# Optimization experiments

Measured on AMD Instinct MI355X. Metric: run time of the kernel, lower is better.

## Reference

```python
import jax, jax.numpy as jnp
import numpy as np

EPS = 1e-5  # BatchNorm3d default eps


def conv1x1(x, w, b):
    # x: (b, cin, t, h, w); w: (cout, cin); b: (cout,)
    return jnp.einsum('bcthw,oc->bothw', x, w) + b[None, :, None, None, None]


def batchnorm(x):
    # BatchNorm3d(affine=False), training mode: per-channel batch stats over (B,T,H,W)
    mean = jnp.mean(x, axis=(0, 2, 3, 4), keepdims=True)
    var = jnp.var(x, axis=(0, 2, 3, 4), keepdims=True)
    return (x - mean) * jax.lax.rsqrt(var + EPS)


def setup_inputs() -> dict:
    key = jax.random.key(0)
    ks = jax.random.split(key, 9)
    B, C, T, H, W = 4, 512, 16, 14, 14
    IC = C // 4
    s_in = 1.0 / np.sqrt(C)
    s_up = 1.0 / np.sqrt(IC)
    return {
        'maps':    jax.random.normal(ks[0], (B, C, T, H, W), jnp.float32),
        'w_theta': jax.random.uniform(ks[1], (IC, C), jnp.float32, -s_in, s_in),
        'b_theta': jax.random.uniform(ks[2], (IC,),   jnp.float32, -s_in, s_in),
        'w_phalt': jax.random.uniform(ks[3], (IC, C), jnp.float32, -s_in, s_in),
        'b_phalt': jax.random.uniform(ks[4], (IC,),   jnp.float32, -s_in, s_in),
        'w_glob':  jax.random.uniform(ks[5], (IC, C), jnp.float32, -s_in, s_in),
        'b_glob':  jax.random.uniform(ks[6], (IC,),   jnp.float32, -s_in, s_in),
        'w_up':    jax.random.uniform(ks[7], (C, IC), jnp.float32, -s_up, s_up),
        'b_up':    jax.random.uniform(ks[8], (C,),    jnp.float32, -s_up, s_up),
    }


def reference(maps, w_theta, b_theta, w_phalt, b_phalt, w_glob, b_glob, w_up, b_up):
    b, c, t, h, w = maps.shape
    ic = c // 4
    n = t * h * w

    theta_maps = batchnorm(conv1x1(maps, w_theta, b_theta))   # (b, ic, t, h, w)
    phalt_maps = batchnorm(conv1x1(maps, w_phalt, b_phalt))   # computed but UNUSED (bug in original)
    global_maps = batchnorm(conv1x1(maps, w_glob, b_glob))

    theta_x = theta_maps.reshape(b, ic, n)                    # (b, ic, n)
    # NOTE: original code uses theta_maps for phalt_x (faithful to source bug)
    relation = jnp.einsum('bcn,bcm->bnm', theta_x, theta_x)   # (b, n, n)
    relation_normalize = jax.nn.softmax(relation / n, axis=-1)

    global_x = global_maps.reshape(b, ic, n)                  # (b, ic, n)
    y = jnp.einsum('bnm,bcm->bcn', relation_normalize, global_x)
    y = y.reshape(b, ic, t, h, w)

    out = conv1x1(y, w_up, b_up) + maps
    return out
```

## Files before the change

kernel.cpp:

```cpp
#include <hip/hip_runtime.h>
#include <hip/hip_bf16.h>


typedef __attribute__((ext_vector_type(8))) short bf16x8;
typedef __attribute__((ext_vector_type(4))) float f32x4;
typedef __attribute__((ext_vector_type(16))) float f32x16;
typedef __attribute__((ext_vector_type(4))) short s16x4;

#define NTOK 3136
#define NELEM 1605632
#define NSPLIT 4

__device__ inline float bf2f(short u) {
    union { unsigned int i; float f; } v;
    v.i = ((unsigned int)(unsigned short)u) << 16;
    return v.f;
}
__device__ inline short f2bf(float x) {
    union { float f; unsigned int i; } v;
    v.f = x;
    unsigned int r = v.i + 0x7FFFu + ((v.i >> 16) & 1u);
    return (short)(r >> 16);
}
__device__ inline unsigned pk2(float lo, float hi) {
    union { float f; unsigned u; } a, b;
    a.f = lo; b.f = hi;
    return __builtin_amdgcn_perm(b.u, a.u, 0x07060302u);
}
__device__ inline void pl32swap(unsigned &a, unsigned &b) {
    asm("v_permlane32_swap_b32 %0, %1" : "+v"(a), "+v"(b));
}
__device__ inline void glds16(const void* g, void* l) {
    __builtin_amdgcn_global_load_lds((const __attribute__((address_space(1))) void*)g,
                                     (__attribute__((address_space(3))) void*)l, 16, 0, 0);
}

__global__ __launch_bounds__(256) void prep_w(const float* __restrict__ wt,
                                              const float* __restrict__ wg,
                                              const float* __restrict__ wup,
                                              short* __restrict__ Wb,
                                              short* __restrict__ wupb)
{
    const int i = blockIdx.x * 256 + threadIdx.x;
    if (i < 131072) {
        const int r = i >> 9;
        const int c = i & 511;
        const float w = (r < 128) ? wt[(size_t)r * 512 + c] : wg[(size_t)(r - 128) * 512 + c];
        Wb[i] = f2bf(w);
    } else {
        const int j = i - 131072;
        wupb[j] = f2bf(wup[j]);
    }
}

__global__ __launch_bounds__(256) void conv_in_f(const float* __restrict__ maps,
                                                 const short* __restrict__ Wb,
                                                 short* __restrict__ Tt,
                                                 short* __restrict__ Gpre,
                                                 float* __restrict__ psum,
                                                 float* __restrict__ psq)
{
    const int nt = blockIdx.x, b = blockIdx.y;
    const int n0 = nt * 32;
    const int t = threadIdx.x;
    const int w = __builtin_amdgcn_readfirstlane(t >> 6);
    const int lane = t & 63;
    const int l15 = lane & 15, lhi = lane >> 4;

    __shared__ short Bt[32][136];

    const float* mp = maps + (size_t)b * 512 * NTOK + n0;
    const int cl = t >> 3;
    const int f4 = t & 7;

    f32x4 acc[4][2];
#pragma unroll
    for (int g = 0; g < 4; g++)
#pragma unroll
        for (int j = 0; j < 2; j++) acc[g][j] = f32x4{0.f, 0.f, 0.f, 0.f};

    f32x4 rg[4];
#pragma unroll
    for (int p = 0; p < 4; p++)
        rg[p] = *(const f32x4*)(mp + (size_t)(p * 32 + cl) * NTOK + f4 * 4);

    for (int kc = 0; kc < 4; kc++) {
        __syncthreads();
#pragma unroll
        for (int p = 0; p < 4; p++) {
            const int cc = p * 32 + cl;
#pragma unroll
            for (int i = 0; i < 4; i++) Bt[f4 * 4 + i][cc] = f2bf(rg[p][i]);
        }
        if (kc < 3) {
#pragma unroll
            for (int p = 0; p < 4; p++)
                rg[p] = *(const f32x4*)(mp + (size_t)((kc + 1) * 128 + p * 32 + cl) * NTOK + f4 * 4);
        }
        __syncthreads();
#pragma unroll
        for (int ks = 0; ks < 4; ks++) {
            bf16x8 af[4], bv[2];
#pragma unroll
            for (int g = 0; g < 4; g++)
                af[g] = *(const bf16x8*)(Wb + (size_t)(w * 64 + g * 16 + l15) * 512 + kc * 128 + ks * 32 + lhi * 8);
#pragma unroll
            for (int j = 0; j < 2; j++)
                bv[j] = *(const bf16x8*)(&Bt[j * 16 + l15][ks * 32 + lhi * 8]);
#pragma unroll
            for (int g = 0; g < 4; g++)
#pragma unroll
                for (int j = 0; j < 2; j++)
                    acc[g][j] = __builtin_amdgcn_mfma_f32_16x16x32_bf16(af[g], bv[j], acc[g][j], 0, 0, 0);
        }
    }

    if (w < 2) {
#pragma unroll
        for (int g = 0; g < 4; g++)
#pragma unroll
            for (int j = 0; j < 2; j++) {
                s16x4 v;
#pragma unroll
                for (int r = 0; r < 4; r++) v[r] = f2bf(acc[g][j][r]);
                *(s16x4*)(Tt + ((size_t)b * NTOK + n0 + j * 16 + l15) * 128 + w * 64 + g * 16 + lhi * 4) = v;
            }
    } else {
#pragma unroll
        for (int g = 0; g < 4; g++)
#pragma unroll
            for (int j = 0; j < 2; j++)
#pragma unroll
                for (int r = 0; r < 4; r++) {
                    const int icg = (w - 2) * 64 + g * 16 + lhi * 4 + r;
                    Gpre[((size_t)b * 128 + icg) * NTOK + n0 + j * 16 + l15] = f2bf(acc[g][j][r]);
                }
    }
#pragma unroll
    for (int g = 0; g < 4; g++)
#pragma unroll
        for (int r = 0; r < 4; r++) {
            float s = acc[g][0][r] + acc[g][1][r];
            float q = acc[g][0][r] * acc[g][0][r] + acc[g][1][r] * acc[g][1][r];
#pragma unroll
            for (int off = 1; off < 16; off <<= 1) {
                s += __shfl_xor(s, off);
                q += __shfl_xor(q, off);
            }
            if (l15 == 0) {
                const int ch = w * 64 + g * 16 + lhi * 4 + r;
                psum[(size_t)ch * 392 + b * 98 + nt] = s;
                psq [(size_t)ch * 392 + b * 98 + nt] = q;
            }
        }
}

__global__ __launch_bounds__(64) void stats_fin(const float* __restrict__ psum,
                                                const float* __restrict__ psq,
                                                float* __restrict__ st)
{
    const int ch = blockIdx.x;
    const int lane = threadIdx.x;
    float s = 0.f, q = 0.f;
    for (int i = lane; i < 392; i += 64) {
        s += psum[(size_t)ch * 392 + i];
        q += psq [(size_t)ch * 392 + i];
    }
#pragma unroll
    for (int off = 32; off; off >>= 1) { s += __shfl_xor(s, off); q += __shfl_xor(q, off); }
    if (lane == 0) {
        const float mean = s / 12544.f;
        const float var = q / 12544.f - mean * mean;
        st[ch] = mean;
        st[256 + ch] = rsqrtf(var + 1e-5f);
    }
}

__global__ __launch_bounds__(256, 2) void attn_k(const short* __restrict__ Tt,
                                                 const short* __restrict__ Gpre,
                                                 const float* __restrict__ st,
                                                 short* __restrict__ Opart,
                                                 float* __restrict__ dpart)
{
    constexpr int N = NTOK;
    const int b = blockIdx.y, s = blockIdx.z;
    const int w = __builtin_amdgcn_readfirstlane(threadIdx.x >> 6);
    const int lane = threadIdx.x & 63;
    const int l31 = lane & 31, hi = lane >> 5;
    const int q0w = blockIdx.x * 128 + w * 32;

    __shared__ __align__(16) short Kl[2][64][128];
    __shared__ __align__(16) short Vl[2][128][64];

    const short* tb = Tt + (size_t)b * N * 128;
    const short* gb = Gpre + (size_t)b * 128 * N;

    const float kexp = 1.44269504089f / (float)N;
    bf16x8 qf[8];
    {
        int row = q0w + l31; row = row < N ? row : N - 1;
        const short* qp = tb + (size_t)row * 128;
#pragma unroll
        for (int ks = 0; ks < 8; ks++) {
            const int c0 = ks * 16 + hi * 8;
            const bf16x8 v = *(const bf16x8*)(qp + c0);
            const f32x4 mA = *(const f32x4*)(st + c0);
            const f32x4 mB = *(const f32x4*)(st + c0 + 4);
            const f32x4 rA = *(const f32x4*)(st + 256 + c0);
            const f32x4 rB = *(const f32x4*)(st + 256 + c0 + 4);
            bf16x8 q;
#pragma unroll
            for (int j = 0; j < 4; j++) q[j] = f2bf((bf2f(v[j]) - mA[j]) * (rA[j] * rA[j] * kexp));
#pragma unroll
            for (int j = 0; j < 4; j++) q[4 + j] = f2bf((bf2f(v[4 + j]) - mB[j]) * (rB[j] * rB[j] * kexp));
            qf[ks] = q;
        }
    }

    f32x16 accv[4];
#pragma unroll
    for (int it = 0; it < 4; it++)
#pragma unroll
        for (int r = 0; r < 16; r++) accv[it][r] = 0.f;
    float denom = 0.f;

    auto STAGE = [&](int bufi, int m0) {
#pragma unroll
        for (int i = 0; i < 4; i++) {
            const int rb = w * 16 + i * 4;
            const int krow = rb + (lane >> 4);
            const int ls = (lane & 15) ^ (krow & 7);
            glds16(tb + (size_t)(m0 + krow) * 128 + ls * 8, (void*)&Kl[bufi][rb][0]);
        }
#pragma unroll
        for (int i = 0; i < 4; i++) {
            const int rb = w * 32 + i * 8;
            const int vrow = rb + (lane >> 3);
            const int ls = (lane & 7) ^ (vrow & 7);
            glds16(gb + (size_t)vrow * N + m0 + ls * 8, (void*)&Vl[bufi][rb][0]);
        }
    };

    const int nt = (49 - s + NSPLIT - 1) / NSPLIT;
    int mt = s;
    STAGE(0, mt * 64);
    __syncthreads();
    int buf = 0;

    const int fr = (l31 & 7) << 4;

    auto mkpa = [&](const f32x16 &sv, bf16x8 *dst) {
        float e[16];
#pragma unroll
        for (int r = 0; r < 16; r++) { e[r] = exp2f(sv[r]); denom += e[r]; }
        unsigned c0 = pk2(e[0], e[1]),  c1 = pk2(e[2], e[3]);
        unsigned c2 = pk2(e[4], e[5]),  c3 = pk2(e[6], e[7]);
        unsigned c4 = pk2(e[8], e[9]),  c5 = pk2(e[10], e[11]);
        unsigned c6 = pk2(e[12], e[13]), c7 = pk2(e[14], e[15]);
        pl32swap(c0, c2); pl32swap(c1, c3); pl32swap(c4, c6); pl32swap(c5, c7);
        union U { unsigned u[4]; bf16x8 v; } f0, f1;
        f0.u[0] = c0; f0.u[1] = c1; f0.u[2] = c2; f0.u[3] = c3;
        f1.u[0] = c4; f1.u[1] = c5; f1.u[2] = c6; f1.u[3] = c7;
        dst[0] = f0.v; dst[1] = f1.v;
    };

    for (int t = 0; t < nt; ++t) {
        if (t + 1 < nt) STAGE(buf ^ 1, (mt + NSPLIT) * 64);

        f32x16 sv0, sv1;
#pragma unroll
        for (int r = 0; r < 16; r++) { sv0[r] = 0.f; sv1[r] = 0.f; }
        __builtin_amdgcn_s_setprio(1);
#pragma unroll
        for (int ks = 0; ks < 8; ks++) {
            const int co = (ks * 32 + hi * 16) ^ fr;
            bf16x8 kf0 = *(const bf16x8*)((const char*)&Kl[buf][l31][0] + co);
            bf16x8 kf1 = *(const bf16x8*)((const char*)&Kl[buf][32 + l31][0] + co);
            sv0 = __builtin_amdgcn_mfma_f32_32x32x16_bf16(kf0, qf[ks], sv0, 0, 0, 0);
            sv1 = __builtin_amdgcn_mfma_f32_32x32x16_bf16(kf1, qf[ks], sv1, 0, 0, 0);
        }
        __builtin_amdgcn_s_setprio(0);

        bf16x8 pa[4];
        mkpa(sv0, &pa[0]);
        mkpa(sv1, &pa[2]);

        __builtin_amdgcn_s_setprio(1);
#pragma unroll
        for (int kp = 0; kp < 4; kp++) {
            const int cv = kp * 32 + hi * 16;
#pragma unroll
            for (int it = 0; it < 4; it++) {
                const int row = it * 32 + l31;
                bf16x8 vf = *(const bf16x8*)((const char*)&Vl[buf][row][0] + (cv ^ fr));
                accv[it] = __builtin_amdgcn_mfma_f32_32x32x16_bf16(pa[kp], vf, accv[it], 0, 0, 0);
            }
        }
        __builtin_amdgcn_s_setprio(0);
        __syncthreads();
        buf ^= 1;
        mt += NSPLIT;
    }

    denom += __shfl_xor(denom, 32);

    short* op = Opart + ((size_t)(s * 4 + b)) * N * 128;
#pragma unroll
    for (int it = 0; it < 4; it++)
#pragma unroll
        for (int r = 0; r < 16; r++) {
            const int n = q0w + (r & 3) + 8 * (r >> 2) + 4 * hi;
            if (n < N) op[(size_t)n * 128 + it * 32 + l31] = f2bf(accv[it][r]);
        }
    if (lane < 32) {
        const int n = q0w + l31;
        if (n < N) dpart[(size_t)(s * 4 + b) * N + n] = denom;
    }
}

__global__ __launch_bounds__(256) void conv_out_f(const short* __restrict__ Opart,
                                                  const float* __restrict__ dpart,
                                                  const float* __restrict__ st,
                                                  const short* __restrict__ wupb,
                                                  const float* __restrict__ bup,
                                                  const float* __restrict__ maps,
                                                  float* __restrict__ out)
{
    const int n0 = blockIdx.x * 32, b = blockIdx.y;
    const int t = threadIdx.x;

    __shared__ float denl[32];
    __shared__ __align__(16) short Yl[32][128];

    if (t < 32) {
        float d = 0.f;
#pragma unroll
        for (int s = 0; s < NSPLIT; s++) d += dpart[(size_t)(s * 4 + b) * NTOK + n0 + t];
        denl[t] = 1.0f / d;
    }
    __syncthreads();

#pragma unroll
    for (int g = 0; g < 2; g++) {
        const int e = t + g * 256;
        const int nl = e >> 4, icg = (e & 15) * 8;
        const float rdn = denl[nl];
        float sum[8] = {0.f, 0.f, 0.f, 0.f, 0.f, 0.f, 0.f, 0.f};
#pragma unroll
        for (int s = 0; s < NSPLIT; s++) {
            const size_t base = ((size_t)(s * 4 + b) * NTOK + n0 + nl) * 128 + icg;
            const bf16x8 a = *(const bf16x8*)(Opart + base);
#pragma unroll
            for (int j = 0; j < 8; j++) sum[j] += bf2f(a[j]);
        }
        const f32x4 mA = *(const f32x4*)(st + 128 + icg);
        const f32x4 mB = *(const f32x4*)(st + 128 + icg + 4);
        const f32x4 rA = *(const f32x4*)(st + 384 + icg);
        const f32x4 rB = *(const f32x4*)(st + 384 + icg + 4);
        s16x4 v0, v1;
#pragma unroll
        for (int j = 0; j < 4; j++) v0[j] = f2bf((sum[j] * rdn - mA[j]) * rA[j]);
#pragma unroll
        for (int j = 0; j < 4; j++) v1[j] = f2bf((sum[4 + j] * rdn - mB[j]) * rB[j]);
        char* ybase = (char*)&Yl[nl][0];
        const int sw = (nl & 7) << 4;
        *(s16x4*)(ybase + ((icg * 2) ^ sw)) = v0;
        *(s16x4*)(ybase + (((icg * 2) ^ sw) + 8)) = v1;
    }
    __syncthreads();

    const int wv = __builtin_amdgcn_readfirstlane(t >> 6);
    const int lane = t & 63;
    const int l15 = lane & 15, lhi = lane >> 4;
    const int c0 = wv * 128;
    const int fY = (l15 & 7) << 4;

    f32x4 acc[8][2];
#pragma unroll
    for (int g = 0; g < 8; g++)
#pragma unroll
        for (int j = 0; j < 2; j++) acc[g][j] = f32x4{0.f, 0.f, 0.f, 0.f};

#pragma unroll
    for (int ks = 0; ks < 4; ks++) {
        bf16x8 af[8], bv[2];
#pragma unroll
        for (int g = 0; g < 8; g++)
            af[g] = *(const bf16x8*)(wupb + (size_t)(c0 + g * 16 + l15) * 128 + ks * 32 + lhi * 8);
#pragma unroll
        for (int j = 0; j < 2; j++)
            bv[j] = *(const bf16x8*)((const char*)&Yl[j * 16 + l15][0] + ((ks * 64 + lhi * 16) ^ fY));
#pragma unroll
        for (int g = 0; g < 8; g++)
#pragma unroll
            for (int j = 0; j < 2; j++)
                acc[g][j] = __builtin_amdgcn_mfma_f32_16x16x32_bf16(af[g], bv[j], acc[g][j], 0, 0, 0);
    }
#pragma unroll
    for (int g = 0; g < 8; g++)
#pragma unroll
        for (int j = 0; j < 2; j++)
#pragma unroll
            for (int r = 0; r < 4; r++) {
                const int c = c0 + g * 16 + lhi * 4 + r;
                const int n = n0 + j * 16 + l15;
                const size_t o = ((size_t)b * 512 + c) * NTOK + n;
                out[o] = acc[g][j][r] + bup[c] + maps[o];
            }
}

extern "C" void kernel_launch(void* const* d_in, const int* in_sizes, int n_in,
                              void* d_out, int out_size, void* d_ws, size_t ws_size,
                              hipStream_t stream)
{
    const float* maps    = (const float*)d_in[0];
    const float* w_theta = (const float*)d_in[1];
    const float* w_glob  = (const float*)d_in[5];
    const float* w_up    = (const float*)d_in[7];
    const float* b_up    = (const float*)d_in[8];
    float* out = (float*)d_out;

    short* Tt    = (short*)d_ws;
    short* Gpre  = Tt + NELEM;
    short* Wb    = Gpre + NELEM;
    short* wupb  = Wb + 131072;
    float* st    = (float*)(wupb + 65536);
    float* psum  = st + 512;
    float* psq   = psum + 100352;
    float* dpart = psq + 100352;
    short* Opart = (short*)(dpart + 50176);

    prep_w    <<<768,             256, 0, stream>>>(w_theta, w_glob, w_up, Wb, wupb);
    conv_in_f <<<dim3(98, 4),     256, 0, stream>>>(maps, Wb, Tt, Gpre, psum, psq);
    stats_fin <<<256,             64,  0, stream>>>(psum, psq, st);
    attn_k    <<<dim3(25, 4, NSPLIT), 256, 0, stream>>>(Tt, Gpre, st, Opart, dpart);
    conv_out_f<<<dim3(98, 4),     256, 0, stream>>>(Opart, dpart, st, wupb, b_up, maps, out);
}
```

Baseline: 90.05 us.

## Raise attention split count to seven with 32-key tiles and higher occupancy

The attention kernel now processes 32-key tiles instead of 64 and splits the key range across 7 partitions instead of 4, each running a fixed 14 iterations. This raises the grid from 400 to 700 blocks. Halving the LDS tiles lets launch bounds target 4 blocks per SM instead of 2. The V-tile swizzle is reworked for the narrower rows, and the setprio hints are dropped. The denominator partials now reuse the psum buffer to make workspace room for more output partials, at the cost of more partial data for the output conv to reduce.

```diff
diff --git a/kernel.cpp b/kernel.cpp
--- a/kernel.cpp
+++ b/kernel.cpp
@@ -9,7 +9,7 @@
 
 #define NTOK 3136
 #define NELEM 1605632
-#define NSPLIT 4
+#define NSPLIT 7
 
 __device__ inline float bf2f(short u) {
     union { unsigned int i; float f; } v;
@@ -176,7 +176,7 @@
     }
 }
 
-__global__ __launch_bounds__(256, 2) void attn_k(const short* __restrict__ Tt,
+__global__ __launch_bounds__(256, 4) void attn_k(const short* __restrict__ Tt,
                                                  const short* __restrict__ Gpre,
                                                  const float* __restrict__ st,
                                                  short* __restrict__ Opart,
@@ -189,8 +189,8 @@
     const int l31 = lane & 31, hi = lane >> 5;
     const int q0w = blockIdx.x * 128 + w * 32;
 
-    __shared__ __align__(16) short Kl[2][64][128];
-    __shared__ __align__(16) short Vl[2][128][64];
+    __shared__ __align__(16) short Kl[2][32][128];
+    __shared__ __align__(16) short Vl[2][128][32];
 
     const short* tb = Tt + (size_t)b * N * 128;
     const short* gb = Gpre + (size_t)b * 128 * N;
@@ -226,28 +226,28 @@
 
     auto STAGE = [&](int bufi, int m0) {
 #pragma unroll
-        for (int i = 0; i < 4; i++) {
-            const int rb = w * 16 + i * 4;
+        for (int i = 0; i < 2; i++) {
+            const int rb = w * 8 + i * 4;
             const int krow = rb + (lane >> 4);
             const int ls = (lane & 15) ^ (krow & 7);
             glds16(tb + (size_t)(m0 + krow) * 128 + ls * 8, (void*)&Kl[bufi][rb][0]);
         }
 #pragma unroll
-        for (int i = 0; i < 4; i++) {
-            const int rb = w * 32 + i * 8;
-            const int vrow = rb + (lane >> 3);
-            const int ls = (lane & 7) ^ (vrow & 7);
+        for (int i = 0; i < 2; i++) {
+            const int rb = w * 32 + i * 16;
+            const int vrow = rb + (lane >> 2);
+            const int ls = (lane & 3) ^ ((vrow >> 1) & 3);
             glds16(gb + (size_t)vrow * N + m0 + ls * 8, (void*)&Vl[bufi][rb][0]);
         }
     };
 
-    const int nt = (49 - s + NSPLIT - 1) / NSPLIT;
     int mt = s;
-    STAGE(0, mt * 64);
+    STAGE(0, mt * 32);
     __syncthreads();
     int buf = 0;
 
-    const int fr = (l31 & 7) << 4;
+    const int frk = (l31 & 7) << 4;
+    const int frv = ((l31 >> 1) & 3) << 4;
 
     auto mkpa = [&](const f32x16 &sv, bf16x8 *dst) {
         float e[16];
@@ -264,39 +264,31 @@
         dst[0] = f0.v; dst[1] = f1.v;
     };
 
-    for (int t = 0; t < nt; ++t) {
-        if (t + 1 < nt) STAGE(buf ^ 1, (mt + NSPLIT) * 64);
-
-        f32x16 sv0, sv1;
-#pragma unroll
-        for (int r = 0; r < 16; r++) { sv0[r] = 0.f; sv1[r] = 0.f; }
-        __builtin_amdgcn_s_setprio(1);
+    for (int t = 0; t < 14; ++t) {
+        if (t + 1 < 14) STAGE(buf ^ 1, (mt + NSPLIT) * 32);
+
+        f32x16 sv0;
+#pragma unroll
+        for (int r = 0; r < 16; r++) sv0[r] = 0.f;
 #pragma unroll
         for (int ks = 0; ks < 8; ks++) {
-            const int co = (ks * 32 + hi * 16) ^ fr;
+            const int co = (ks * 32 + hi * 16) ^ frk;
             bf16x8 kf0 = *(const bf16x8*)((const char*)&Kl[buf][l31][0] + co);
-            bf16x8 kf1 = *(const bf16x8*)((const char*)&Kl[buf][32 + l31][0] + co);
             sv0 = __builtin_amdgcn_mfma_f32_32x32x16_bf16(kf0, qf[ks], sv0, 0, 0, 0);
-            sv1 = __builtin_amdgcn_mfma_f32_32x32x16_bf16(kf1, qf[ks], sv1, 0, 0, 0);
-        }
-        __builtin_amdgcn_s_setprio(0);
-
-        bf16x8 pa[4];
-        mkpa(sv0, &pa[0]);
-        mkpa(sv1, &pa[2]);
-
-        __builtin_amdgcn_s_setprio(1);
-#pragma unroll
-        for (int kp = 0; kp < 4; kp++) {
+        }
+
+        bf16x8 pa[2];
+        mkpa(sv0, pa);
+
+#pragma unroll
+        for (int kp = 0; kp < 2; kp++) {
             const int cv = kp * 32 + hi * 16;
 #pragma unroll
             for (int it = 0; it < 4; it++) {
-                const int row = it * 32 + l31;
-                bf16x8 vf = *(const bf16x8*)((const char*)&Vl[buf][row][0] + (cv ^ fr));
+                bf16x8 vf = *(const bf16x8*)((const char*)&Vl[buf][it * 32 + l31][0] + (cv ^ frv));
                 accv[it] = __builtin_amdgcn_mfma_f32_32x32x16_bf16(pa[kp], vf, accv[it], 0, 0, 0);
             }
         }
-        __builtin_amdgcn_s_setprio(0);
         __syncthreads();
         buf ^= 1;
         mt += NSPLIT;
@@ -427,8 +419,8 @@
     float* st    = (float*)(wupb + 65536);
     float* psum  = st + 512;
     float* psq   = psum + 100352;
-    float* dpart = psq + 100352;
-    short* Opart = (short*)(dpart + 50176);
+    float* dpart = psum;
+    short* Opart = (short*)(psq + 100352);
 
     prep_w    <<<768,             256, 0, stream>>>(w_theta, w_glob, w_up, Wb, wupb);
     conv_in_f <<<dim3(98, 4),     256, 0, stream>>>(maps, Wb, Tt, Gpre, psum, psq);
```

Result: slower. 108.1 us (+20.1%).
